# Optimization experiments

Hardware: AMD Instinct MI355X
Metric: run time of the kernel (lower is better)

Reference implementation:

```python
import jax, jax.numpy as jnp
import numpy as np

B, T, C, H, N, FFN = 4, 1024, 2048, 32, 64, 7168
HEAD_DIVISOR = 8.0
EPS = 1e-5


def setup_inputs() -> dict:
    key = jax.random.key(0)
    ks = jax.random.split(key, 30)
    rn = lambda k, s, sc=0.02: jax.random.normal(k, s, jnp.float32) * sc
    ru = lambda k, s: jax.random.uniform(k, s, jnp.float32)
    return {
        "x": jax.random.normal(ks[0], (B, T, C), jnp.float32),
        "att_shift": jax.random.normal(ks[1], (B, C), jnp.float32),
        "wkv_state": jax.random.normal(ks[2], (B, H, N, N), jnp.float32) * 0.1,
        "ffn_shift": jax.random.normal(ks[3], (B, C), jnp.float32),
        "ln1_w": jnp.ones((C,), jnp.float32), "ln1_b": jnp.zeros((C,), jnp.float32),
        "ln2_w": jnp.ones((C,), jnp.float32), "ln2_b": jnp.zeros((C,), jnp.float32),
        "mix_k": ru(ks[4], (C,)), "mix_v": ru(ks[5], (C,)),
        "mix_r": ru(ks[6], (C,)), "mix_g": ru(ks[7], (C,)),
        "Wr": rn(ks[8], (C, C)), "Wk": rn(ks[9], (C, C)), "Wv": rn(ks[10], (C, C)),
        "Wg": rn(ks[11], (C, C)), "Wo": rn(ks[12], (C, C)),
        "time_decay": jax.random.normal(ks[13], (H, N), jnp.float32) * 0.5,
        "time_faaaa": jax.random.normal(ks[14], (H, N), jnp.float32) * 0.1,
        "gn_w": jnp.ones((C,), jnp.float32), "gn_b": jnp.zeros((C,), jnp.float32),
        "cmix_k": ru(ks[15], (C,)), "cmix_r": ru(ks[16], (C,)),
        "Wck": rn(ks[17], (C, FFN)), "Wcr": rn(ks[18], (C, C)), "Wcv": rn(ks[19], (FFN, C)),
    }


def _ln(z, w, b):
    m = z.mean(-1, keepdims=True)
    v = z.var(-1, keepdims=True)
    return (z - m) / jnp.sqrt(v + EPS) * w + b


def _shift(x, shift_state):
    # prepend carried last-token state, drop final position
    return jnp.concatenate([shift_state[:, None, :], x[:, :-1]], axis=1)


def reference(x, att_shift, wkv_state, ffn_shift, ln1_w, ln1_b, ln2_w, ln2_b,
              mix_k, mix_v, mix_r, mix_g, Wr, Wk, Wv, Wg, Wo,
              time_decay, time_faaaa, gn_w, gn_b, cmix_k, cmix_r, Wck, Wcr, Wcv):
    Bb, Tt, Cc = x.shape

    # ---- TimeMix ----
    x1 = _ln(x, ln1_w, ln1_b)
    xx = _shift(x1, att_shift)
    xk = x1 * mix_k + xx * (1 - mix_k)
    xv = x1 * mix_v + xx * (1 - mix_v)
    xr = x1 * mix_r + xx * (1 - mix_r)
    xg = x1 * mix_g + xx * (1 - mix_g)
    r = (xr @ Wr).reshape(Bb, Tt, H, N)
    k = (xk @ Wk).reshape(Bb, Tt, H, N)
    v = (xv @ Wv).reshape(Bb, Tt, H, N)
    g = jax.nn.silu(xg @ Wg)

    w = jnp.exp(-jnp.exp(time_decay))[None, :, :, None]  # [1,H,N,1] decay on k-index
    u = time_faaaa[None, :, :, None]                      # [1,H,N,1] bonus on current token

    def step(S, rkv):  # S: [B,H,N,N] (k-index i, v-index j)
        rr, kk, vv = rkv
        kv = kk[..., :, None] * vv[..., None, :]          # [B,H,N,N]
        y = jnp.einsum('bhi,bhij->bhj', rr, S + u * kv)
        return S * w + kv, y

    rkv = (jnp.moveaxis(r, 1, 0), jnp.moveaxis(k, 1, 0), jnp.moveaxis(v, 1, 0))
    new_wkv, ys = jax.lax.scan(step, wkv_state, rkv)      # ys: [T,B,H,N]
    att = jnp.moveaxis(ys, 0, 1)                          # [B,T,H,N]

    # GroupNorm(n_head groups) on att / head_size_divisor
    z = att / HEAD_DIVISOR
    m = z.mean(-1, keepdims=True)
    var = z.var(-1, keepdims=True)
    z = (z - m) / jnp.sqrt(var + EPS)
    z = z * gn_w.reshape(H, N) + gn_b.reshape(H, N)
    att_out = (z.reshape(Bb, Tt, Cc) * g) @ Wo

    x = x + att_out

    # ---- ChannelMix ----
    x2 = _ln(x, ln2_w, ln2_b)
    xx2 = _shift(x2, ffn_shift)
    xck = x2 * cmix_k + xx2 * (1 - cmix_k)
    xcr = x2 * cmix_r + xx2 * (1 - cmix_r)
    kk = jnp.square(jax.nn.relu(xck @ Wck))
    kv = kk @ Wcv
    ffn_out = jax.nn.sigmoid(xcr @ Wcr) * kv
    x = x + ffn_out

    return x, x1[:, -1], new_wkv, x2[:, -1]
```

## Files before the change

kernel.cpp:

```cpp
#include <hip/hip_runtime.h>
#include <cstdint>
#include <cstddef>

typedef unsigned short u16;
typedef unsigned int u32;
typedef short bf16x8 __attribute__((ext_vector_type(8)));
typedef unsigned short u16x4 __attribute__((ext_vector_type(4)));
typedef unsigned short u16x8 __attribute__((ext_vector_type(8)));
typedef float f32x4 __attribute__((ext_vector_type(4)));

#define DEV __device__ __forceinline__

constexpr int Bb = 4, Tt = 1024, Cc = 2048, Hh = 32, Nd = 64, FF = 7168;
constexpr int BT = Bb * Tt;
constexpr int NCH = 16;

DEV u16 f2bf(float f) {
  union { float f; unsigned u; } un; un.f = f;
  unsigned r = un.u + 0x7FFFu + ((un.u >> 16) & 1u);
  return (u16)(r >> 16);
}
DEV float bf2f(u16 h) {
  union { unsigned u; float f; } un; un.u = ((unsigned)h) << 16;
  return un.f;
}
DEV void gll16(const u16* gp, u16* lp) {
  __builtin_amdgcn_global_load_lds(
      (const __attribute__((address_space(1))) unsigned int*)gp,
      (__attribute__((address_space(3))) unsigned int*)lp,
      16, 0, 0);
}
DEV int xcd_swz(int f, int nwg) {
  int q = nwg >> 3;
  return (f & 7) * q + (f >> 3);
}

DEV void transp64_body(const float* __restrict__ W, u16* __restrict__ Wt,
                       int Kk, int Nn) {
  const int n0 = blockIdx.x * 64, k0 = blockIdx.y * 64;
  const int tx = threadIdx.x & 15, ty = threadIdx.x >> 4;
  const int kk = k0 + ty * 4, nn = n0 + tx * 4;
  const float* p = W + (size_t)kk * Nn + nn;
  f32x4 r0 = *(const f32x4*)(p);
  f32x4 r1 = *(const f32x4*)(p + (size_t)Nn);
  f32x4 r2 = *(const f32x4*)(p + 2 * (size_t)Nn);
  f32x4 r3 = *(const f32x4*)(p + 3 * (size_t)Nn);
  #pragma unroll
  for (int j = 0; j < 4; j++) {
    u16x4 o;
    o[0] = f2bf(r0[j]); o[1] = f2bf(r1[j]); o[2] = f2bf(r2[j]); o[3] = f2bf(r3[j]);
    *(u16x4*)(Wt + (size_t)(nn + j) * Kk + kk) = o;
  }
}

__global__ void transp64(const float* __restrict__ W, u16* __restrict__ Wt,
                         int Kk, int Nn) {
  transp64_body(W, Wt, Kk, Nn);
}

__global__ void transp64_6cc(const float* __restrict__ W0, const float* __restrict__ W1,
                             const float* __restrict__ W2, const float* __restrict__ W3,
                             const float* __restrict__ W4, const float* __restrict__ W5,
                             u16* __restrict__ T0, u16* __restrict__ T1,
                             u16* __restrict__ T2, u16* __restrict__ T3,
                             u16* __restrict__ T4, u16* __restrict__ T5) {
  const int z = blockIdx.z;
  const float* W = (z == 0) ? W0 : (z == 1) ? W1 : (z == 2) ? W2 :
                   (z == 3) ? W3 : (z == 4) ? W4 : W5;
  u16* T = (z == 0) ? T0 : (z == 1) ? T1 : (z == 2) ? T2 :
           (z == 3) ? T3 : (z == 4) ? T4 : T5;
  transp64_body(W, T, Cc, Cc);
}

DEV void block_ln(const float* __restrict__ src, int tid, float* red,
                  float vals[8], float& mean, float& inv) {
  float s = 0.f, ss = 0.f;
  #pragma unroll
  for (int i = 0; i < 8; i++) {
    float t = src[tid + i * 256];
    vals[i] = t; s += t; ss += t * t;
  }
  #pragma unroll
  for (int m = 1; m < 64; m <<= 1) { s += __shfl_xor(s, m); ss += __shfl_xor(ss, m); }
  int lane = tid & 63, wv = tid >> 6;
  __syncthreads();
  if (lane == 0) { red[wv] = s; red[4 + wv] = ss; }
  __syncthreads();
  s = red[0] + red[1] + red[2] + red[3];
  ss = red[4] + red[5] + red[6] + red[7];
  mean = s * (1.f / Cc);
  float var = ss * (1.f / Cc) - mean * mean;
  inv = rsqrtf(var + 1e-5f);
}

__global__ __launch_bounds__(256)
void ln_mix4(const float* __restrict__ x, const float* __restrict__ shift,
             const float* __restrict__ w, const float* __restrict__ b,
             const float* __restrict__ mk, const float* __restrict__ mv,
             const float* __restrict__ mr, const float* __restrict__ mg,
             u16* __restrict__ xk, u16* __restrict__ xv,
             u16* __restrict__ xr, u16* __restrict__ xg,
             float* __restrict__ last) {
  int row = blockIdx.x;
  int t = row & (Tt - 1), bb = row >> 10;
  int tid = threadIdx.x;
  __shared__ float red[8];
  const float* cur = x + (size_t)row * Cc;
  float cv[8], pv[8], cm, ci, pm = 0.f, pi = 1.f;
  block_ln(cur, tid, red, cv, cm, ci);
  bool t0 = (t == 0);
  const float* prev = t0 ? (shift + (size_t)bb * Cc) : (cur - Cc);
  if (!t0) {
    block_ln(prev, tid, red, pv, pm, pi);
  } else {
    #pragma unroll
    for (int i = 0; i < 8; i++) pv[i] = prev[tid + i * 256];
  }
  size_t o = (size_t)row * Cc;
  bool isLast = (t == Tt - 1);
  #pragma unroll
  for (int i = 0; i < 8; i++) {
    int c = tid + i * 256;
    float xc = (cv[i] - cm) * ci * w[c] + b[c];
    float xp = t0 ? pv[i] : (pv[i] - pm) * pi * w[c] + b[c];
    xk[o + c] = f2bf(xp + mk[c] * (xc - xp));
    xv[o + c] = f2bf(xp + mv[c] * (xc - xp));
    xr[o + c] = f2bf(xp + mr[c] * (xc - xp));
    xg[o + c] = f2bf(xp + mg[c] * (xc - xp));
    if (isLast) last[(size_t)bb * Cc + c] = xc;
  }
}

__global__ __launch_bounds__(256)
void ln_mix2(const float* __restrict__ x, const float* __restrict__ shift,
             const float* __restrict__ w, const float* __restrict__ b,
             const float* __restrict__ ck, const float* __restrict__ cr,
             u16* __restrict__ xck, u16* __restrict__ xcr,
             float* __restrict__ last) {
  int row = blockIdx.x;
  int t = row & (Tt - 1), bb = row >> 10;
  int tid = threadIdx.x;
  __shared__ float red[8];
  const float* cur = x + (size_t)row * Cc;
  float cv[8], pv[8], cm, ci, pm = 0.f, pi = 1.f;
  block_ln(cur, tid, red, cv, cm, ci);
  bool t0 = (t == 0);
  const float* prev = t0 ? (shift + (size_t)bb * Cc) : (cur - Cc);
  if (!t0) {
    block_ln(prev, tid, red, pv, pm, pi);
  } else {
    #pragma unroll
    for (int i = 0; i < 8; i++) pv[i] = prev[tid + i * 256];
  }
  size_t o = (size_t)row * Cc;
  bool isLast = (t == Tt - 1);
  #pragma unroll
  for (int i = 0; i < 8; i++) {
    int c = tid + i * 256;
    float xc = (cv[i] - cm) * ci * w[c] + b[c];
    float xp = t0 ? pv[i] : (pv[i] - pm) * pi * w[c] + b[c];
    xck[o + c] = f2bf(xp + ck[c] * (xc - xp));
    xcr[o + c] = f2bf(xp + cr[c] * (xc - xp));
    if (isLast) last[(size_t)bb * Cc + c] = xc;
  }
}

DEV int swz32(int row, int off) {
  return (row << 6) + (off ^ ((((row >> 1) & 1) << 4) | (((row >> 2) & 1) << 5)));
}

DEV void stageA32(const u16* __restrict__ g, int ldK, u16* slot, int tid) {
  #pragma unroll
  for (int p = 0; p < 2; p++) {
    const int D = p * 8192 + tid * 16;
    const int row = D >> 6;
    const int off = (D & 63) ^ ((((row >> 1) & 1) << 4) | (((row >> 2) & 1) << 5));
    gll16(g + (size_t)row * ldK + (off >> 1), (u16*)((char*)slot + D));
  }
}
DEV void stageB32(const u16* __restrict__ g, int ldK, u16* slot, int tid) {
  const int D = tid * 16;
  const int row = D >> 6;
  const int off = (D & 63) ^ ((((row >> 1) & 1) << 4) | (((row >> 2) & 1) << 5));
  gll16(g + (size_t)row * ldK + (off >> 1), (u16*)((char*)slot + D));
}

template <int EPI>
DEV void gemm_core(const u16* __restrict__ A, const u16* __restrict__ Bt,
                   int N, int K, int ldK,
                   float* __restrict__ Co, u16* __restrict__ Cb,
                   const float* __restrict__ X1, const float* __restrict__ X2,
                   const u16* __restrict__ X2b,
                   u16 (*lA)[8192], u16 (*lB)[4096],
                   int m0, int n0, int act) {
  const int tid = threadIdx.x;
  const int w = tid >> 6, lane = tid & 63;
  const int l15 = lane & 15, l4 = lane >> 4;
  const int wm = (w & 3) * 64, wn = (w >> 2) * 64;
  const int nt = K >> 5;

  const u16* Ag = A + (size_t)m0 * ldK;
  const u16* Bg = Bt + (size_t)n0 * ldK;

  f32x4 acc[4][4] = {};

  stageA32(Ag, ldK, lA[0], tid);
  stageB32(Bg, ldK, lB[0], tid);
  asm volatile("s_waitcnt vmcnt(0)" ::: "memory");
  asm volatile("s_barrier" ::: "memory");

  for (int t = 0; t < nt; t++) {
    const int cur = t & 1;
    if (t + 1 < nt) {
      stageA32(Ag + (size_t)(t + 1) * 32, ldK, lA[cur ^ 1], tid);
      stageB32(Bg + (size_t)(t + 1) * 32, ldK, lB[cur ^ 1], tid);
    }
    bf16x8 a[4], b[4];
    #pragma unroll
    for (int mf = 0; mf < 4; mf++)
      a[mf] = *(const bf16x8*)((char*)lA[cur] + swz32(wm + mf * 16 + l15, l4 * 16));
    #pragma unroll
    for (int nf = 0; nf < 4; nf++)
      b[nf] = *(const bf16x8*)((char*)lB[cur] + swz32(wn + nf * 16 + l15, l4 * 16));
    __builtin_amdgcn_s_setprio(1);
    #pragma unroll
    for (int mf = 0; mf < 4; mf++)
      #pragma unroll
      for (int nf = 0; nf < 4; nf++)
        acc[mf][nf] = __builtin_amdgcn_mfma_f32_16x16x32_bf16(
            a[mf], b[nf], acc[mf][nf], 0, 0, 0);
    __builtin_amdgcn_s_setprio(0);
    if (t + 1 < nt) asm volatile("s_waitcnt vmcnt(0)" ::: "memory");
    asm volatile("s_barrier" ::: "memory");
  }

  #pragma unroll
  for (int mf = 0; mf < 4; mf++) {
    #pragma unroll
    for (int reg = 0; reg < 4; reg++) {
      const int gr = m0 + wm + mf * 16 + l4 * 4 + reg;
      const size_t ro = (size_t)gr * N;
      #pragma unroll
      for (int nf = 0; nf < 4; nf++) {
        const int gc = n0 + wn + nf * 16 + l15;
        float val = acc[mf][nf][reg];
        if constexpr (EPI == 0) {
          Co[ro + gc] = val;
        } else if constexpr (EPI == 1) {
          if (act) val = val / (1.f + __expf(-val));
          Cb[ro + gc] = f2bf(val);
        } else if constexpr (EPI == 3) {
          float tr = fmaxf(val, 0.f);
          Cb[ro + gc] = f2bf(tr * tr);
        } else if constexpr (EPI == 4) {
          Co[ro + gc] = X1[ro + gc] + val;
        } else {
          float s = 1.f / (1.f + __expf(-val));
          float kvv = X2[ro + gc] + bf2f(X2b[ro + gc]);
          Co[ro + gc] = fmaf(s, kvv, X1[ro + gc]);
        }
      }
    }
  }
}

template <int EPI>
__global__ __launch_bounds__(512, 4)
void gemmN(const u16* __restrict__ A, const u16* __restrict__ Bt,
           int N, int K,
           float* __restrict__ Co, u16* __restrict__ Cb,
           const float* __restrict__ X1, const float* __restrict__ X2,
           const u16* __restrict__ X2b, int NX) {
  __shared__ __align__(16) u16 lA[2][8192];
  __shared__ __align__(16) u16 lB[2][4096];
  int o = xcd_swz(blockIdx.x, gridDim.x);
  int xb = o % NX, yb = o / NX;
  gemm_core<EPI>(A, Bt, N, K, K, Co, Cb, X1, X2, X2b, lA, lB,
                 yb * 256, xb * 128, 0);
}

__global__ __launch_bounds__(512, 4)
void gemm_proj(const u16* __restrict__ A0, const u16* __restrict__ A1,
               const u16* __restrict__ A2, const u16* __restrict__ A3,
               const u16* __restrict__ B0, const u16* __restrict__ B1,
               const u16* __restrict__ B2, const u16* __restrict__ B3,
               u16* __restrict__ C0, u16* __restrict__ C1,
               u16* __restrict__ C2, u16* __restrict__ C3) {
  __shared__ __align__(16) u16 lA[2][8192];
  __shared__ __align__(16) u16 lB[2][4096];
  int o = xcd_swz(blockIdx.x, gridDim.x);
  int xb = o & 15, yb = (o >> 4) & 15, z = o >> 8;
  const u16* A = (z == 0) ? A0 : (z == 1) ? A1 : (z == 2) ? A2 : A3;
  const u16* Bt = (z == 0) ? B0 : (z == 1) ? B1 : (z == 2) ? B2 : B3;
  u16* Cb = (z == 0) ? C0 : (z == 1) ? C1 : (z == 2) ? C2 : C3;
  gemm_core<1>(A, Bt, Cc, Cc, Cc, nullptr, Cb, nullptr, nullptr, nullptr,
               lA, lB, yb * 256, xb * 128, z == 3);
}

__global__ __launch_bounds__(512, 4)
void gemm_splitk(const u16* __restrict__ A, const u16* __restrict__ Bt,
                 float* __restrict__ kv0, u16* __restrict__ kv1) {
  __shared__ __align__(16) u16 lA[2][8192];
  __shared__ __align__(16) u16 lB[2][4096];
  int o = xcd_swz(blockIdx.x, gridDim.x);
  int xb = o & 15, yb = (o >> 4) & 15, z = o >> 8;
  const int Koff = z * (FF / 2);
  if (z == 0)
    gemm_core<0>(A + Koff, Bt + Koff, Cc, FF / 2, FF, kv0, nullptr,
                 nullptr, nullptr, nullptr, lA, lB, yb * 256, xb * 128, 0);
  else
    gemm_core<1>(A + Koff, Bt + Koff, Cc, FF / 2, FF, nullptr, kv1,
                 nullptr, nullptr, nullptr, lA, lB, yb * 256, xb * 128, 0);
}

__global__ __launch_bounds__(256)
void wkv_pre(const u16* __restrict__ rg, const u16* __restrict__ kg,
             const u16* __restrict__ vg, const float* __restrict__ td,
             const float* __restrict__ tf,
             float* __restrict__ Yb, float* __restrict__ Db,
             u16* __restrict__ Rtb) {
  __shared__ float Pt[64][68];
  __shared__ float uL[64];
  __shared__ u16 rB[64 * 72];
  __shared__ u16 kB[64 * 72];
  __shared__ u16 Rh[64 * 72];
  __shared__ u16 KhX[96 * 72];
  __shared__ u16 vA[64 * 72];
  __shared__ u16 Vt[64 * 72];

  const int tid = threadIdx.x, bid = blockIdx.x;
  const int bh = bid >> 4, c = bid & 15;
  const int b = bh >> 5, h = bh & 31;
  const int lane = tid & 63, w = tid >> 6;

  {
    int i = tid & 63;
    float d = __expf(td[h * 64 + i]);
    float c1 = -1.4426950408889634f * d;
    int e0 = (tid >> 6) * 16;
    #pragma unroll
    for (int e = 0; e < 16; e++) Pt[e0 + e][i] = exp2f(c1 * (float)(e0 + e));
    if (tid < 64) uL[tid] = tf[h * 64 + tid];
  }
  __syncthreads();

  const int row = tid >> 2, col0 = (tid & 3) * 16;
  const int tl = row & 15;
  {
    size_t gro = ((size_t)b * Tt + c * 64 + row) * Cc + h * 64 + col0;
    u16x8 rv0 = *(const u16x8*)(rg + gro);
    u16x8 rv1 = *(const u16x8*)(rg + gro + 8);
    u16x8 kv0 = *(const u16x8*)(kg + gro);
    u16x8 kv1 = *(const u16x8*)(kg + gro + 8);
    u16x8 vv0 = *(const u16x8*)(vg + gro);
    u16x8 vv1 = *(const u16x8*)(vg + gro + 8);
    *(u16x8*)&rB[row * 72 + col0] = rv0; *(u16x8*)&rB[row * 72 + col0 + 8] = rv1;
    *(u16x8*)&kB[row * 72 + col0] = kv0; *(u16x8*)&kB[row * 72 + col0 + 8] = kv1;
    *(u16x8*)&vA[row * 72 + col0] = vv0; *(u16x8*)&vA[row * 72 + col0 + 8] = vv1;
    float rf[16], kf[16];
    #pragma unroll
    for (int e = 0; e < 8; e++) { rf[e] = bf2f(rv0[e]); rf[8 + e] = bf2f(rv1[e]); }
    #pragma unroll
    for (int e = 0; e < 8; e++) { kf[e] = bf2f(kv0[e]); kf[8 + e] = bf2f(kv1[e]); }
    u16x8 o0, o1, t0_, t1_;
    #pragma unroll
    for (int e = 0; e < 8; e++) {
      o0[e] = f2bf(rf[e] * Pt[tl][col0 + e]);
      o1[e] = f2bf(rf[8 + e] * Pt[tl][col0 + 8 + e]);
      t0_[e] = f2bf(rf[e] * Pt[row][col0 + e]);
      t1_[e] = f2bf(rf[8 + e] * Pt[row][col0 + 8 + e]);
    }
    *(u16x8*)&Rh[row * 72 + col0] = o0; *(u16x8*)&Rh[row * 72 + col0 + 8] = o1;
    u16* rtp = Rtb + (size_t)bid * 4096 + row * 64 + col0;
    *(u16x8*)rtp = t0_; *(u16x8*)(rtp + 8) = t1_;
    if (row < 48) {
      u16x8 a0, a1;
      #pragma unroll
      for (int e = 0; e < 8; e++) {
        a0[e] = f2bf(kf[e] * Pt[15 - tl][col0 + e]);
        a1[e] = f2bf(kf[8 + e] * Pt[15 - tl][col0 + 8 + e]);
      }
      *(u16x8*)&KhX[row * 72 + col0] = a0; *(u16x8*)&KhX[row * 72 + col0 + 8] = a1;
    }
    if (row < 32) {
      u16x8 a0, a1;
      #pragma unroll
      for (int e = 0; e < 8; e++) {
        a0[e] = f2bf(kf[e] * Pt[31 - tl][col0 + e]);
        a1[e] = f2bf(kf[8 + e] * Pt[31 - tl][col0 + 8 + e]);
      }
      *(u16x8*)&KhX[(48 + row) * 72 + col0] = a0; *(u16x8*)&KhX[(48 + row) * 72 + col0 + 8] = a1;
    }
    if (row < 16) {
      u16x8 a0, a1;
      #pragma unroll
      for (int e = 0; e < 8; e++) {
        a0[e] = f2bf(kf[e] * Pt[47 - tl][col0 + e]);
        a1[e] = f2bf(kf[8 + e] * Pt[47 - tl][col0 + 8 + e]);
      }
      *(u16x8*)&KhX[(80 + row) * 72 + col0] = a0; *(u16x8*)&KhX[(80 + row) * 72 + col0 + 8] = a1;
    }
  }
  __syncthreads();

  {
    const int jj = tid & 63, s0 = (tid >> 6) * 16;
    #pragma unroll
    for (int ds = 0; ds < 16; ds += 2) {
      u32 pk = ((u32)vA[(s0 + ds + 1) * 72 + jj] << 16) | vA[(s0 + ds) * 72 + jj];
      *(u32*)&Vt[jj * 72 + s0 + ds] = pk;
    }
  }
  __syncthreads();

  u16* aB = vA;
  {
    const int pr[6] = {1, 2, 3, 2, 3, 3};
    const int qr[6] = {0, 1, 2, 0, 1, 0};
    const int dr[6] = {0, 0, 0, 1, 1, 2};
    const int lr = lane & 15, kq = lane >> 4;
    for (int pi = w; pi < 6; pi += 4) {
      const int p = pr[pi], q = qr[pi], d = dr[pi];
      const int kbase = (d == 0) ? q * 16 : (d == 1) ? 48 + q * 16 : 80 + q * 16;
      f32x4 aacc = {};
      #pragma unroll
      for (int kf2 = 0; kf2 < 2; kf2++) {
        bf16x8 af = *(const bf16x8*)&Rh[(p * 16 + lr) * 72 + kf2 * 32 + kq * 8];
        bf16x8 bf_ = *(const bf16x8*)&KhX[(kbase + lr) * 72 + kf2 * 32 + kq * 8];
        aacc = __builtin_amdgcn_mfma_f32_16x16x32_bf16(af, bf_, aacc, 0, 0, 0);
      }
      #pragma unroll
      for (int reg = 0; reg < 4; reg++) {
        aB[(p * 16 + kq * 4 + reg) * 72 + q * 16 + lr] = f2bf(aacc[reg]);
        aB[(q * 16 + kq * 4 + reg) * 72 + p * 16 + lr] = 0;
      }
    }
    for (int e = lane; e < 256; e += 64) {
      const int tl2 = e >> 4, sl = e & 15;
      float a = 0.f;
      if (sl <= tl2) {
        const u16* rp = &rB[(w * 16 + tl2) * 72];
        const u16* kp = &kB[(w * 16 + sl) * 72];
        const float* pp = (sl == tl2) ? uL : &Pt[tl2 - 1 - sl][0];
        #pragma unroll
        for (int i0 = 0; i0 < 64; i0 += 4) {
          u16x4 ra = *(const u16x4*)(rp + i0);
          u16x4 ka = *(const u16x4*)(kp + i0);
          f32x4 pa = *(const f32x4*)(pp + i0);
          #pragma unroll
          for (int di = 0; di < 4; di++)
            a = fmaf(bf2f(ra[di]) * bf2f(ka[di]), pa[di], a);
        }
      }
      aB[(w * 16 + tl2) * 72 + w * 16 + sl] = f2bf(a);
    }
  }
  __syncthreads();

  u16* Ktt = KhX;
  {
    const int ii = tid & 63, s0 = (tid >> 6) * 16;
    #pragma unroll
    for (int ds = 0; ds < 16; ds += 2) {
      float v0 = bf2f(kB[(s0 + ds) * 72 + ii]) * Pt[63 - (s0 + ds)][ii];
      float v1 = bf2f(kB[(s0 + ds + 1) * 72 + ii]) * Pt[63 - (s0 + ds + 1)][ii];
      u32 pk = ((u32)f2bf(v1) << 16) | f2bf(v0);
      *(u32*)&Ktt[ii * 72 + s0 + ds] = pk;
    }
  }
  __syncthreads();

  const int lr = lane & 15, kq = lane >> 4;
  {
    f32x4 yac[4] = {};
    #pragma unroll
    for (int kf2 = 0; kf2 < 2; kf2++) {
      bf16x8 af = *(const bf16x8*)&aB[(w * 16 + lr) * 72 + kf2 * 32 + kq * 8];
      #pragma unroll
      for (int nf = 0; nf < 4; nf++) {
        bf16x8 bf_ = *(const bf16x8*)&Vt[(nf * 16 + lr) * 72 + kf2 * 32 + kq * 8];
        yac[nf] = __builtin_amdgcn_mfma_f32_16x16x32_bf16(af, bf_, yac[nf], 0, 0, 0);
      }
    }
    float* Yp = Yb + (size_t)bid * 4096;
    #pragma unroll
    for (int nf = 0; nf < 4; nf++)
      #pragma unroll
      for (int reg = 0; reg < 4; reg++)
        Yp[(w * 16 + kq * 4 + reg) * 64 + nf * 16 + lr] = yac[nf][reg];

    f32x4 dac[4] = {};
    #pragma unroll
    for (int kf2 = 0; kf2 < 2; kf2++) {
      bf16x8 af = *(const bf16x8*)&Ktt[(w * 16 + lr) * 72 + kf2 * 32 + kq * 8];
      #pragma unroll
      for (int nf = 0; nf < 4; nf++) {
        bf16x8 bf_ = *(const bf16x8*)&Vt[(nf * 16 + lr) * 72 + kf2 * 32 + kq * 8];
        dac[nf] = __builtin_amdgcn_mfma_f32_16x16x32_bf16(af, bf_, dac[nf], 0, 0, 0);
      }
    }
    float* Dp = Db + (size_t)bid * 4096;
    #pragma unroll
    for (int nf = 0; nf < 4; nf++)
      #pragma unroll
      for (int reg = 0; reg < 4; reg++)
        Dp[(w * 16 + kq * 4 + reg) * 64 + nf * 16 + lr] = dac[nf][reg];
  }
}

__global__ __launch_bounds__(256)
void wkv_scan(const float* __restrict__ s0g, const float* __restrict__ td,
              const float* __restrict__ Db, u16* __restrict__ Sbb,
              float* __restrict__ sout) {
  const int bh = blockIdx.x, h = bh & 31;
  const int tid = threadIdx.x;
  const int i = tid >> 2, j0 = (tid & 3) * 16;
  float d = __expf(td[h * 64 + i]);
  float w64 = exp2f(-1.4426950408889634f * d * 64.f);
  f32x4 S[4];
  const float* sp = s0g + ((size_t)bh * 64 + i) * 64 + j0;
  #pragma unroll
  for (int q = 0; q < 4; q++) S[q] = *(const f32x4*)(sp + q * 4);
  for (int c = 0; c < NCH; c++) {
    u16* op = Sbb + ((size_t)(bh * 16 + c)) * 4096 + i * 64 + j0;
    u16x8 o0, o1;
    #pragma unroll
    for (int e = 0; e < 4; e++) { o0[e] = f2bf(S[0][e]); o0[4 + e] = f2bf(S[1][e]);
                                  o1[e] = f2bf(S[2][e]); o1[4 + e] = f2bf(S[3][e]); }
    *(u16x8*)op = o0; *(u16x8*)(op + 8) = o1;
    const float* dp = Db + ((size_t)(bh * 16 + c)) * 4096 + i * 64 + j0;
    #pragma unroll
    for (int q = 0; q < 4; q++) {
      f32x4 dv = *(const f32x4*)(dp + q * 4);
      #pragma unroll
      for (int e = 0; e < 4; e++) S[q][e] = fmaf(w64, S[q][e], dv[e]);
    }
  }
  float* fo = sout + ((size_t)bh * 64 + i) * 64 + j0;
  #pragma unroll
  for (int q = 0; q < 4; q++) *(f32x4*)(fo + q * 4) = S[q];
}

__global__ __launch_bounds__(256)
void wkv_post(const u16* __restrict__ Rtb, const u16* __restrict__ Sbb,
              const float* __restrict__ Yb, const u16* __restrict__ g,
              const float* __restrict__ gnw, const float* __restrict__ gnb,
              u16* __restrict__ xo) {
  __shared__ u16 Rt[64 * 72];
  __shared__ u16 St[64 * 72];
  __shared__ u16 xoL[64 * 72];
  const int tid = threadIdx.x, bid = blockIdx.x;
  const int bh = bid >> 4, c = bid & 15;
  const int b = bh >> 5, h = bh & 31;
  const int lane = tid & 63, w = tid >> 6;
  const int row = tid >> 2, col0 = (tid & 3) * 16;

  {
    const u16* rp = Rtb + (size_t)bid * 4096 + row * 64 + col0;
    u16x8 a0 = *(const u16x8*)rp, a1 = *(const u16x8*)(rp + 8);
    *(u16x8*)&Rt[row * 72 + col0] = a0; *(u16x8*)&Rt[row * 72 + col0 + 8] = a1;
  }
  {
    const u16* sp = Sbb + ((size_t)(bh * 16 + c)) * 4096 + row * 64 + col0;
    u16x8 s0 = *(const u16x8*)sp, s1 = *(const u16x8*)(sp + 8);
    #pragma unroll
    for (int e = 0; e < 8; e++) {
      St[(col0 + e) * 72 + row] = s0[e];
      St[(col0 + 8 + e) * 72 + row] = s1[e];
    }
  }
  const int lr = lane & 15, kq = lane >> 4;
  f32x4 acc[4];
  {
    const float* Yp = Yb + (size_t)bid * 4096;
    #pragma unroll
    for (int nf = 0; nf < 4; nf++)
      #pragma unroll
      for (int reg = 0; reg < 4; reg++)
        acc[nf][reg] = Yp[(w * 16 + kq * 4 + reg) * 64 + nf * 16 + lr];
  }
  __syncthreads();
  #pragma unroll
  for (int kf2 = 0; kf2 < 2; kf2++) {
    bf16x8 af = *(const bf16x8*)&Rt[(w * 16 + lr) * 72 + kf2 * 32 + kq * 8];
    #pragma unroll
    for (int nf = 0; nf < 4; nf++) {
      bf16x8 bf_ = *(const bf16x8*)&St[(nf * 16 + lr) * 72 + kf2 * 32 + kq * 8];
      acc[nf] = __builtin_amdgcn_mfma_f32_16x16x32_bf16(af, bf_, acc[nf], 0, 0, 0);
    }
  }
  #pragma unroll
  for (int reg = 0; reg < 4; reg++) {
    float s = 0.f, ss = 0.f;
    #pragma unroll
    for (int nf = 0; nf < 4; nf++) {
      float z = acc[nf][reg] * 0.125f;
      s += z; ss += z * z;
    }
    #pragma unroll
    for (int m = 1; m < 16; m <<= 1) { s += __shfl_xor(s, m); ss += __shfl_xor(ss, m); }
    float mean = s * (1.f / 64.f);
    float var = ss * (1.f / 64.f) - mean * mean;
    float inv = rsqrtf(var + 1e-5f);
    const int tau = w * 16 + kq * 4 + reg;
    #pragma unroll
    for (int nf = 0; nf < 4; nf++) {
      const int col = nf * 16 + lr;
      float z = acc[nf][reg] * 0.125f;
      float zn = (z - mean) * inv * gnw[h * 64 + col] + gnb[h * 64 + col];
      float gv = bf2f(g[((size_t)b * Tt + c * 64 + tau) * Cc + h * 64 + col]);
      xoL[tau * 72 + col] = f2bf(zn * gv);
    }
  }
  __syncthreads();
  {
    u16x8 o0 = *(const u16x8*)&xoL[row * 72 + col0];
    u16x8 o1 = *(const u16x8*)&xoL[row * 72 + col0 + 8];
    u16* xop = xo + ((size_t)b * Tt + c * 64 + row) * Cc + h * 64 + col0;
    *(u16x8*)xop = o0; *(u16x8*)(xop + 8) = o1;
  }
}

extern "C" void kernel_launch(void* const* d_in, const int* in_sizes, int n_in,
                              void* d_out, int out_size, void* d_ws, size_t ws_size,
                              hipStream_t stream) {
  const float* x         = (const float*)d_in[0];
  const float* att_shift = (const float*)d_in[1];
  const float* wkv0      = (const float*)d_in[2];
  const float* ffn_shift = (const float*)d_in[3];
  const float* ln1w = (const float*)d_in[4];
  const float* ln1b = (const float*)d_in[5];
  const float* ln2w = (const float*)d_in[6];
  const float* ln2b = (const float*)d_in[7];
  const float* mixk = (const float*)d_in[8];
  const float* mixv = (const float*)d_in[9];
  const float* mixr = (const float*)d_in[10];
  const float* mixg = (const float*)d_in[11];
  const float* Wr = (const float*)d_in[12];
  const float* Wk = (const float*)d_in[13];
  const float* Wv = (const float*)d_in[14];
  const float* Wg = (const float*)d_in[15];
  const float* Wo = (const float*)d_in[16];
  const float* td = (const float*)d_in[17];
  const float* tf = (const float*)d_in[18];
  const float* gnw = (const float*)d_in[19];
  const float* gnb = (const float*)d_in[20];
  const float* cmk = (const float*)d_in[21];
  const float* cmr = (const float*)d_in[22];
  const float* Wck = (const float*)d_in[23];
  const float* Wcr = (const float*)d_in[24];
  const float* Wcv = (const float*)d_in[25];

  constexpr size_t SZ_CC = (size_t)Cc * Cc * 2;
  constexpr size_t SZ_CF = (size_t)Cc * FF * 2;
  constexpr size_t SZ_AB = (size_t)BT * Cc * 2;
  constexpr size_t O_W   = 0;
  constexpr size_t O_R1  = 6 * SZ_CC + 2 * SZ_CF;
  constexpr size_t R1_SZ = 4 * SZ_AB;
  constexpr size_t O_R2  = O_R1 + R1_SZ;
  constexpr size_t R2_SZ = 3 * SZ_AB;
  constexpr size_t O_R3  = O_R2 + R2_SZ;
  constexpr size_t WS_NEED = O_R3 + SZ_AB;

  if (ws_size < WS_NEED) return;

  char* ws = (char*)d_ws;
  u16* WrT  = (u16*)(ws + O_W);
  u16* WkT  = (u16*)(ws + O_W + 1 * SZ_CC);
  u16* WvT  = (u16*)(ws + O_W + 2 * SZ_CC);
  u16* WgT  = (u16*)(ws + O_W + 3 * SZ_CC);
  u16* WoT  = (u16*)(ws + O_W + 4 * SZ_CC);
  u16* WcrT = (u16*)(ws + O_W + 5 * SZ_CC);
  u16* WckT = (u16*)(ws + O_W + 6 * SZ_CC);
  u16* WcvT = (u16*)(ws + O_W + 6 * SZ_CC + SZ_CF);

  u16*   xk  = (u16*)(ws + O_R1);
  u16*   xv  = (u16*)(ws + O_R1 + SZ_AB);
  u16*   xr  = (u16*)(ws + O_R1 + 2 * SZ_AB);
  u16*   xg  = (u16*)(ws + O_R1 + 3 * SZ_AB);
  float* Yb  = (float*)(ws + O_R1);
  u16*   Rtb = (u16*)(ws + O_R1 + 2 * SZ_AB);
  u16*   Sbb = (u16*)(ws + O_R1 + 3 * SZ_AB);
  u16*   kk  = (u16*)(ws + O_R1);
  u16*   rb  = (u16*)(ws + O_R2);
  u16*   kb  = (u16*)(ws + O_R2 + SZ_AB);
  u16*   vb  = (u16*)(ws + O_R2 + 2 * SZ_AB);
  u16*   xcr = (u16*)(ws + O_R2);
  u16*   xck = (u16*)(ws + O_R2 + SZ_AB);
  u16*   xo  = (u16*)(ws + O_R2 + 2 * SZ_AB);
  float* kv0 = (float*)(ws + O_R2 + SZ_AB);
  u16*   gbuf = (u16*)(ws + O_R3);
  u16*   kv1  = (u16*)(ws + O_R3);

  float* out      = (float*)d_out;
  float* x1_last  = out + (size_t)BT * Cc;
  float* wkv_out  = x1_last + (size_t)Bb * Cc;
  float* x2_last  = wkv_out + (size_t)Bb * Hh * Nd * Nd;
  float* Db       = out;

  transp64_6cc<<<dim3(32, 32, 6), 256, 0, stream>>>(Wr, Wk, Wv, Wg, Wo, Wcr,
                                                    WrT, WkT, WvT, WgT, WoT, WcrT);
  transp64<<<dim3(112, 32), 256, 0, stream>>>(Wck, WckT, Cc, FF);
  transp64<<<dim3(32, 112), 256, 0, stream>>>(Wcv, WcvT, FF, Cc);

  ln_mix4<<<BT, 256, 0, stream>>>(x, att_shift, ln1w, ln1b,
                                  mixk, mixv, mixr, mixg, xk, xv, xr, xg, x1_last);
  gemm_proj<<<1024, 512, 0, stream>>>(xr, xk, xv, xg,
                                      WrT, WkT, WvT, WgT,
                                      rb, kb, vb, gbuf);
  wkv_pre<<<Bb * Hh * NCH, 256, 0, stream>>>(rb, kb, vb, td, tf, Yb, Db, Rtb);
  wkv_scan<<<Bb * Hh, 256, 0, stream>>>(wkv0, td, Db, Sbb, wkv_out);
  wkv_post<<<Bb * Hh * NCH, 256, 0, stream>>>(Rtb, Sbb, Yb, gbuf, gnw, gnb, xo);
  gemmN<4><<<256, 512, 0, stream>>>(xo, WoT, Cc, Cc, out, nullptr, x,
                                    nullptr, nullptr, 16);
  ln_mix2<<<BT, 256, 0, stream>>>(out, ffn_shift, ln2w, ln2b, cmk, cmr, xck, xcr, x2_last);
  gemmN<3><<<896, 512, 0, stream>>>(xck, WckT, FF, Cc, nullptr, kk,
                                    nullptr, nullptr, nullptr, 56);
  gemm_splitk<<<512, 512, 0, stream>>>(kk, WcvT, kv0, kv1);
  gemmN<6><<<256, 512, 0, stream>>>(xcr, WcrT, Cc, Cc, out, nullptr, out,
                                    kv0, kv1, 16);

  (void)in_sizes; (void)n_in; (void)out_size;
}
```

Measured before the change: 760.6 us.

## Use 256x256 GEMM tiles with triple-buffered LDS prefetch pipeline

Generalizes the GEMM core to support 256x256 block tiles (each wave computes 64x128) for the projection, FFN-up and split-K FFN-down GEMMs, halving block counts and raising arithmetic intensity per block. Also switches from double to triple buffering with a two-stage-ahead prefetch and partial vmcnt waits, so global loads overlap more compute. Costs are more accumulator registers (128 floats per lane), larger LDS footprint (up to 96KB per block), removal of the occupancy hint, and fewer blocks, which can hurt load balance on 256 CUs.

```diff
diff --git a/kernel.cpp b/kernel.cpp
--- a/kernel.cpp
+++ b/kernel.cpp
@@ -168,70 +168,90 @@
 DEV int swz32(int row, int off) {
   return (row << 6) + (off ^ ((((row >> 1) & 1) << 4) | (((row >> 2) & 1) << 5)));
 }
-
-DEV void stageA32(const u16* __restrict__ g, int ldK, u16* slot, int tid) {
+DEV void stage16k(const u16* __restrict__ g, int ldK, char* slot, int tid) {
   #pragma unroll
   for (int p = 0; p < 2; p++) {
     const int D = p * 8192 + tid * 16;
     const int row = D >> 6;
     const int off = (D & 63) ^ ((((row >> 1) & 1) << 4) | (((row >> 2) & 1) << 5));
-    gll16(g + (size_t)row * ldK + (off >> 1), (u16*)((char*)slot + D));
-  }
-}
-DEV void stageB32(const u16* __restrict__ g, int ldK, u16* slot, int tid) {
+    gll16(g + (size_t)row * ldK + (off >> 1), (u16*)(slot + D));
+  }
+}
+DEV void stage8k(const u16* __restrict__ g, int ldK, char* slot, int tid) {
   const int D = tid * 16;
   const int row = D >> 6;
   const int off = (D & 63) ^ ((((row >> 1) & 1) << 4) | (((row >> 2) & 1) << 5));
-  gll16(g + (size_t)row * ldK + (off >> 1), (u16*)((char*)slot + D));
-}
-
-template <int EPI>
-DEV void gemm_core(const u16* __restrict__ A, const u16* __restrict__ Bt,
+  gll16(g + (size_t)row * ldK + (off >> 1), (u16*)(slot + D));
+}
+
+template <int EPI, int NB>
+DEV void g256_core(const u16* __restrict__ A, const u16* __restrict__ Bt,
                    int N, int K, int ldK,
                    float* __restrict__ Co, u16* __restrict__ Cb,
                    const float* __restrict__ X1, const float* __restrict__ X2,
                    const u16* __restrict__ X2b,
-                   u16 (*lA)[8192], u16 (*lB)[4096],
-                   int m0, int n0, int act) {
+                   u16* lA, u16* lB, int m0, int n0, int act) {
   const int tid = threadIdx.x;
   const int w = tid >> 6, lane = tid & 63;
   const int l15 = lane & 15, l4 = lane >> 4;
-  const int wm = (w & 3) * 64, wn = (w >> 2) * 64;
+  const int wm = (w & 3) * 64;
+  const int wn = (w >> 2) * (NB * 64);
   const int nt = K >> 5;
+  constexpr int ASL = 8192;
+  constexpr int BSL = NB * 4096;
 
   const u16* Ag = A + (size_t)m0 * ldK;
   const u16* Bg = Bt + (size_t)n0 * ldK;
 
-  f32x4 acc[4][4] = {};
-
-  stageA32(Ag, ldK, lA[0], tid);
-  stageB32(Bg, ldK, lB[0], tid);
-  asm volatile("s_waitcnt vmcnt(0)" ::: "memory");
+  f32x4 acc[4][NB * 4] = {};
+
+  stage16k(Ag, ldK, (char*)lA, tid);
+  if constexpr (NB == 2) stage16k(Bg, ldK, (char*)lB, tid);
+  else                   stage8k(Bg, ldK, (char*)lB, tid);
+  if (nt > 1) {
+    stage16k(Ag + 32, ldK, (char*)(lA + ASL), tid);
+    if constexpr (NB == 2) stage16k(Bg + 32, ldK, (char*)(lB + BSL), tid);
+    else                   stage8k(Bg + 32, ldK, (char*)(lB + BSL), tid);
+    if constexpr (NB == 2) asm volatile("s_waitcnt vmcnt(4)" ::: "memory");
+    else                   asm volatile("s_waitcnt vmcnt(3)" ::: "memory");
+  } else {
+    asm volatile("s_waitcnt vmcnt(0)" ::: "memory");
+  }
   asm volatile("s_barrier" ::: "memory");
 
+  int s0 = 0;
   for (int t = 0; t < nt; t++) {
-    const int cur = t & 1;
-    if (t + 1 < nt) {
-      stageA32(Ag + (size_t)(t + 1) * 32, ldK, lA[cur ^ 1], tid);
-      stageB32(Bg + (size_t)(t + 1) * 32, ldK, lB[cur ^ 1], tid);
-    }
-    bf16x8 a[4], b[4];
+    int s2 = s0 + 2; if (s2 >= 3) s2 -= 3;
+    if (t + 2 < nt) {
+      stage16k(Ag + (size_t)(t + 2) * 32, ldK, (char*)(lA + s2 * ASL), tid);
+      if constexpr (NB == 2) stage16k(Bg + (size_t)(t + 2) * 32, ldK, (char*)(lB + s2 * BSL), tid);
+      else                   stage8k(Bg + (size_t)(t + 2) * 32, ldK, (char*)(lB + s2 * BSL), tid);
+    }
+    const char* As = (const char*)(lA + s0 * ASL);
+    const char* Bs = (const char*)(lB + s0 * BSL);
+    bf16x8 a[4], b[NB * 4];
     #pragma unroll
     for (int mf = 0; mf < 4; mf++)
-      a[mf] = *(const bf16x8*)((char*)lA[cur] + swz32(wm + mf * 16 + l15, l4 * 16));
-    #pragma unroll
-    for (int nf = 0; nf < 4; nf++)
-      b[nf] = *(const bf16x8*)((char*)lB[cur] + swz32(wn + nf * 16 + l15, l4 * 16));
+      a[mf] = *(const bf16x8*)(As + swz32(wm + mf * 16 + l15, l4 * 16));
+    #pragma unroll
+    for (int nf = 0; nf < NB * 4; nf++)
+      b[nf] = *(const bf16x8*)(Bs + swz32(wn + nf * 16 + l15, l4 * 16));
     __builtin_amdgcn_s_setprio(1);
     #pragma unroll
     for (int mf = 0; mf < 4; mf++)
       #pragma unroll
-      for (int nf = 0; nf < 4; nf++)
+      for (int nf = 0; nf < NB * 4; nf++)
         acc[mf][nf] = __builtin_amdgcn_mfma_f32_16x16x32_bf16(
             a[mf], b[nf], acc[mf][nf], 0, 0, 0);
     __builtin_amdgcn_s_setprio(0);
-    if (t + 1 < nt) asm volatile("s_waitcnt vmcnt(0)" ::: "memory");
+    if (t + 2 < nt) {
+      if constexpr (NB == 2) asm volatile("s_waitcnt vmcnt(4)" ::: "memory");
+      else                   asm volatile("s_waitcnt vmcnt(3)" ::: "memory");
+    } else if (t + 1 < nt) {
+      asm volatile("s_waitcnt vmcnt(0)" ::: "memory");
+    }
     asm volatile("s_barrier" ::: "memory");
+    s0++; if (s0 == 3) s0 = 0;
   }
 
   #pragma unroll
@@ -241,7 +261,7 @@
       const int gr = m0 + wm + mf * 16 + l4 * 4 + reg;
       const size_t ro = (size_t)gr * N;
       #pragma unroll
-      for (int nf = 0; nf < 4; nf++) {
+      for (int nf = 0; nf < NB * 4; nf++) {
         const int gc = n0 + wn + nf * 16 + l15;
         float val = acc[mf][nf][reg];
         if constexpr (EPI == 0) {
@@ -265,52 +285,68 @@
 }
 
 template <int EPI>
-__global__ __launch_bounds__(512, 4)
-void gemmN(const u16* __restrict__ A, const u16* __restrict__ Bt,
-           int N, int K,
-           float* __restrict__ Co, u16* __restrict__ Cb,
-           const float* __restrict__ X1, const float* __restrict__ X2,
-           const u16* __restrict__ X2b, int NX) {
-  __shared__ __align__(16) u16 lA[2][8192];
-  __shared__ __align__(16) u16 lB[2][4096];
+__global__ __launch_bounds__(512)
+void gemm256s(const u16* __restrict__ A, const u16* __restrict__ Bt,
+              int N, int K,
+              float* __restrict__ Co, u16* __restrict__ Cb,
+              const float* __restrict__ X1, int NX) {
+  __shared__ __align__(16) u16 lA[3][8192];
+  __shared__ __align__(16) u16 lB[3][8192];
   int o = xcd_swz(blockIdx.x, gridDim.x);
   int xb = o % NX, yb = o / NX;
-  gemm_core<EPI>(A, Bt, N, K, K, Co, Cb, X1, X2, X2b, lA, lB,
-                 yb * 256, xb * 128, 0);
-}
-
-__global__ __launch_bounds__(512, 4)
-void gemm_proj(const u16* __restrict__ A0, const u16* __restrict__ A1,
-               const u16* __restrict__ A2, const u16* __restrict__ A3,
-               const u16* __restrict__ B0, const u16* __restrict__ B1,
-               const u16* __restrict__ B2, const u16* __restrict__ B3,
-               u16* __restrict__ C0, u16* __restrict__ C1,
-               u16* __restrict__ C2, u16* __restrict__ C3) {
-  __shared__ __align__(16) u16 lA[2][8192];
-  __shared__ __align__(16) u16 lB[2][4096];
+  g256_core<EPI, 2>(A, Bt, N, K, K, Co, Cb, X1, nullptr, nullptr,
+                    &lA[0][0], &lB[0][0], yb * 256, xb * 256, 0);
+}
+
+template <int EPI>
+__global__ __launch_bounds__(512)
+void gemm128s(const u16* __restrict__ A, const u16* __restrict__ Bt,
+              int N, int K,
+              float* __restrict__ Co, u16* __restrict__ Cb,
+              const float* __restrict__ X1, const float* __restrict__ X2,
+              const u16* __restrict__ X2b, int NX) {
+  __shared__ __align__(16) u16 lA[3][8192];
+  __shared__ __align__(16) u16 lB[3][4096];
   int o = xcd_swz(blockIdx.x, gridDim.x);
-  int xb = o & 15, yb = (o >> 4) & 15, z = o >> 8;
+  int xb = o % NX, yb = o / NX;
+  g256_core<EPI, 1>(A, Bt, N, K, K, Co, Cb, X1, X2, X2b,
+                    &lA[0][0], &lB[0][0], yb * 256, xb * 128, 0);
+}
+
+__global__ __launch_bounds__(512)
+void gemm256_proj(const u16* __restrict__ A0, const u16* __restrict__ A1,
+                  const u16* __restrict__ A2, const u16* __restrict__ A3,
+                  const u16* __restrict__ B0, const u16* __restrict__ B1,
+                  const u16* __restrict__ B2, const u16* __restrict__ B3,
+                  u16* __restrict__ C0, u16* __restrict__ C1,
+                  u16* __restrict__ C2, u16* __restrict__ C3) {
+  __shared__ __align__(16) u16 lA[3][8192];
+  __shared__ __align__(16) u16 lB[3][8192];
+  int o = xcd_swz(blockIdx.x, gridDim.x);
+  int xb = o & 7, yb = (o >> 3) & 15, z = o >> 7;
   const u16* A = (z == 0) ? A0 : (z == 1) ? A1 : (z == 2) ? A2 : A3;
   const u16* Bt = (z == 0) ? B0 : (z == 1) ? B1 : (z == 2) ? B2 : B3;
   u16* Cb = (z == 0) ? C0 : (z == 1) ? C1 : (z == 2) ? C2 : C3;
-  gemm_core<1>(A, Bt, Cc, Cc, Cc, nullptr, Cb, nullptr, nullptr, nullptr,
-               lA, lB, yb * 256, xb * 128, z == 3);
-}
-
-__global__ __launch_bounds__(512, 4)
-void gemm_splitk(const u16* __restrict__ A, const u16* __restrict__ Bt,
-                 float* __restrict__ kv0, u16* __restrict__ kv1) {
-  __shared__ __align__(16) u16 lA[2][8192];
-  __shared__ __align__(16) u16 lB[2][4096];
+  g256_core<1, 2>(A, Bt, Cc, Cc, Cc, nullptr, Cb, nullptr, nullptr, nullptr,
+                  &lA[0][0], &lB[0][0], yb * 256, xb * 256, z == 3);
+}
+
+__global__ __launch_bounds__(512)
+void gemm256_splitk(const u16* __restrict__ A, const u16* __restrict__ Bt,
+                    float* __restrict__ kv0, u16* __restrict__ kv1) {
+  __shared__ __align__(16) u16 lA[3][8192];
+  __shared__ __align__(16) u16 lB[3][8192];
   int o = xcd_swz(blockIdx.x, gridDim.x);
-  int xb = o & 15, yb = (o >> 4) & 15, z = o >> 8;
+  int xb = o & 7, yb = (o >> 3) & 15, z = o >> 7;
   const int Koff = z * (FF / 2);
   if (z == 0)
-    gemm_core<0>(A + Koff, Bt + Koff, Cc, FF / 2, FF, kv0, nullptr,
-                 nullptr, nullptr, nullptr, lA, lB, yb * 256, xb * 128, 0);
+    g256_core<0, 2>(A + Koff, Bt + Koff, Cc, FF / 2, FF, kv0, nullptr,
+                    nullptr, nullptr, nullptr, &lA[0][0], &lB[0][0],
+                    yb * 256, xb * 256, 0);
   else
-    gemm_core<1>(A + Koff, Bt + Koff, Cc, FF / 2, FF, nullptr, kv1,
-                 nullptr, nullptr, nullptr, lA, lB, yb * 256, xb * 128, 0);
+    g256_core<1, 2>(A + Koff, Bt + Koff, Cc, FF / 2, FF, nullptr, kv1,
+                    nullptr, nullptr, nullptr, &lA[0][0], &lB[0][0],
+                    yb * 256, xb * 256, 0);
 }
 
 __global__ __launch_bounds__(256)
@@ -705,20 +741,19 @@
 
   ln_mix4<<<BT, 256, 0, stream>>>(x, att_shift, ln1w, ln1b,
                                   mixk, mixv, mixr, mixg, xk, xv, xr, xg, x1_last);
-  gemm_proj<<<1024, 512, 0, stream>>>(xr, xk, xv, xg,
-                                      WrT, WkT, WvT, WgT,
-                                      rb, kb, vb, gbuf);
+  gemm256_proj<<<512, 512, 0, stream>>>(xr, xk, xv, xg,
+                                        WrT, WkT, WvT, WgT,
+                                        rb, kb, vb, gbuf);
   wkv_pre<<<Bb * Hh * NCH, 256, 0, stream>>>(rb, kb, vb, td, tf, Yb, Db, Rtb);
   wkv_scan<<<Bb * Hh, 256, 0, stream>>>(wkv0, td, Db, Sbb, wkv_out);
   wkv_post<<<Bb * Hh * NCH, 256, 0, stream>>>(Rtb, Sbb, Yb, gbuf, gnw, gnb, xo);
-  gemmN<4><<<256, 512, 0, stream>>>(xo, WoT, Cc, Cc, out, nullptr, x,
-                                    nullptr, nullptr, 16);
+  gemm128s<4><<<256, 512, 0, stream>>>(xo, WoT, Cc, Cc, out, nullptr, x,
+                                       nullptr, nullptr, 16);
   ln_mix2<<<BT, 256, 0, stream>>>(out, ffn_shift, ln2w, ln2b, cmk, cmr, xck, xcr, x2_last);
-  gemmN<3><<<896, 512, 0, stream>>>(xck, WckT, FF, Cc, nullptr, kk,
-                                    nullptr, nullptr, nullptr, 56);
-  gemm_splitk<<<512, 512, 0, stream>>>(kk, WcvT, kv0, kv1);
-  gemmN<6><<<256, 512, 0, stream>>>(xcr, WcrT, Cc, Cc, out, nullptr, out,
-                                    kv0, kv1, 16);
+  gemm256s<3><<<448, 512, 0, stream>>>(xck, WckT, FF, Cc, nullptr, kk, nullptr, 28);
+  gemm256_splitk<<<256, 512, 0, stream>>>(kk, WcvT, kv0, kv1);
+  gemm128s<6><<<256, 512, 0, stream>>>(xcr, WcrT, Cc, Cc, out, nullptr, out,
+                                       kv0, kv1, 16);
 
   (void)in_sizes; (void)n_in; (void)out_size;
 }
```

Result: slower. 910.6 us (+19.7%).
